# Optimization experiments

Hardware: AMD Instinct MI355X
Metric: run time of the kernel (lower is better)

Reference implementation:

```python
import jax, jax.numpy as jnp
import numpy as np

N, H, E, D, L = 100000, 20000, 1600000, 64, 3
F = 4 * D  # ffn hidden = out_dim * 4


def _ln(x, g, b, eps=1e-5):
    mu = x.mean(-1, keepdims=True)
    var = ((x - mu) ** 2).mean(-1, keepdims=True)
    return (x - mu) * jax.lax.rsqrt(var + eps) * g + b


def _gconv(x, W, b, src, dst, inv_sqrt_src, inv_sqrt_dst, n_dst):
    # DGL GraphConv, norm='both': D_dst^{-1/2} A D_src^{-1/2} (x W) + b
    h = (x * inv_sqrt_src[:, None]) @ W
    agg = jax.ops.segment_sum(h[src], dst, num_segments=n_dst)
    return agg * inv_sqrt_dst[:, None] + b


def setup_inputs() -> dict:
    key = jax.random.key(0)
    ks = jax.random.split(key, 24)
    s = 0.05
    inp = {
        'node_features': jax.random.normal(ks[0], (N, D), jnp.float32),
        'edge_src': jax.random.randint(ks[1], (E,), 0, N),
        'edge_dst': jax.random.randint(ks[2], (E,), 0, H),
        'n_hyper': H,
        # stacked per-layer params [L, ...]
        'Wn2h': jax.random.normal(ks[3], (L, D, D), jnp.float32) * s,
        'bn2h': jnp.zeros((L, D), jnp.float32),
        'Wh2n': jax.random.normal(ks[4], (L, D, D), jnp.float32) * s,
        'bh2n': jnp.zeros((L, D), jnp.float32),
        'W1': jax.random.normal(ks[5], (L, D, F), jnp.float32) * s,
        'b1': jnp.zeros((L, F), jnp.float32),
        'W2': jax.random.normal(ks[6], (L, F, D), jnp.float32) * s,
        'b2': jnp.zeros((L, D), jnp.float32),
        'g1': jnp.ones((L, D), jnp.float32),
        'be1': jnp.zeros((L, D), jnp.float32),
        'g2': jnp.ones((L, D), jnp.float32),
        'be2': jnp.zeros((L, D), jnp.float32),
        'gF': jnp.ones((D,), jnp.float32),
        'bF': jnp.zeros((D,), jnp.float32),
        'Wo': jax.random.normal(ks[7], (D, D), jnp.float32) * s,
        'bo': jnp.zeros((D,), jnp.float32),
    }
    return inp


def reference(node_features, edge_src, edge_dst, n_hyper, Wn2h, bn2h, Wh2n, bh2n,
              W1, b1, W2, b2, g1, be1, g2, be2, gF, bF, Wo, bo):
    n_nodes = node_features.shape[0]
    ones = jnp.ones(edge_src.shape[0], node_features.dtype)
    deg_node = jnp.clip(jax.ops.segment_sum(ones, edge_src, num_segments=n_nodes), 1.0)
    deg_hyp = jnp.clip(jax.ops.segment_sum(ones, edge_dst, num_segments=n_hyper), 1.0)
    is_node = jax.lax.rsqrt(deg_node)  # node out-degree^{-1/2}
    is_hyp = jax.lax.rsqrt(deg_hyp)    # hyperedge in-degree^{-1/2}

    def step(h, p):
        Wa, ba, Wb, bb, w1, c1, w2, c2, gg1, ee1, gg2, ee2 = p
        # node -> hyperedge conv (unused attention output is overwritten in the original)
        h_hyper = _gconv(h, Wa, ba, edge_src, edge_dst, is_node, is_hyp, n_hyper)
        # hyperedge -> node conv on reversed graph (degrees swap roles)
        h_node = _gconv(h_hyper, Wb, bb, edge_dst, edge_src, is_hyp, is_node, n_nodes)
        h = _ln(h + h_node, gg1, ee1)
        h_ffn = jax.nn.relu(h @ w1 + c1) @ w2 + c2
        h = _ln(h + h_ffn, gg2, ee2)
        return h, None

    h, _ = jax.lax.scan(step, node_features,
                        (Wn2h, bn2h, Wh2n, bh2n, W1, b1, W2, b2, g1, be1, g2, be2))
    h = _ln(h, gF, bF)
    return h @ Wo + bo
```

## Files before the change

kernel.cpp:

```cpp
#include <hip/hip_runtime.h>

#define HYP 20000
#define NLAYER 3
#define NB_H 313
#define NB_N 391
#define PT 4096

typedef __attribute__((ext_vector_type(8))) short short8;
typedef __attribute__((ext_vector_type(4))) float floatx4;

static __device__ __forceinline__ unsigned short f2bf(float f){
  union { float f; unsigned u; } v; v.f = f;
  unsigned r = v.u + 0x7FFF + ((v.u >> 16) & 1);
  return (unsigned short)(r >> 16);
}

__global__ __launch_bounds__(256) void k_hist(const int* __restrict__ src,
    const int* __restrict__ dst, int E, int* __restrict__ bh, int* __restrict__ bn){
  __shared__ int lh[NB_H + NB_N];
  int tid = threadIdx.x;
  for (int i = tid; i < NB_H + NB_N; i += 256) lh[i] = 0;
  __syncthreads();
  for (int i = blockIdx.x*256 + tid; i < E; i += gridDim.x*256){
    atomicAdd(&lh[dst[i] >> 6], 1);
    atomicAdd(&lh[NB_H + (src[i] >> 8)], 1);
  }
  __syncthreads();
  for (int i = tid; i < NB_H; i += 256) if (lh[i]) atomicAdd(&bh[i], lh[i]);
  for (int i = tid; i < NB_N; i += 256) if (lh[NB_H+i]) atomicAdd(&bn[i], lh[NB_H+i]);
}

__global__ __launch_bounds__(256) void k_bscan(const int* __restrict__ bh,
    const int* __restrict__ bn, int* __restrict__ bstart_h, int* __restrict__ gcur_h,
    int* __restrict__ bstart_n, int* __restrict__ gcur_n){
  __shared__ int ssc[4];
  __shared__ int scarry;
  int tid = threadIdx.x, lane = tid & 63, wv = tid >> 6;
  if (tid == 0) scarry = 0;
  __syncthreads();
  for (int base = 0; base < NB_H; base += 256){
    int i = base + tid; int v = (i < NB_H) ? bh[i] : 0; int x = v;
    #pragma unroll
    for (int o = 1; o < 64; o <<= 1){ int t = __shfl_up(x,o,64); if (lane >= o) x += t; }
    if (lane == 63) ssc[wv] = x;
    __syncthreads();
    int add = (wv>0?ssc[0]:0)+(wv>1?ssc[1]:0)+(wv>2?ssc[2]:0);
    int c = scarry;
    if (i < NB_H){ int ex = c + add + x - v; bstart_h[i] = ex; gcur_h[i] = ex; }
    __syncthreads();
    if (tid == 255) scarry = c + ssc[0]+ssc[1]+ssc[2]+ssc[3];
    __syncthreads();
  }
  if (tid == 0){ bstart_h[NB_H] = scarry; scarry = 0; }
  __syncthreads();
  for (int base = 0; base < NB_N; base += 256){
    int i = base + tid; int v = (i < NB_N) ? bn[i] : 0; int x = v;
    #pragma unroll
    for (int o = 1; o < 64; o <<= 1){ int t = __shfl_up(x,o,64); if (lane >= o) x += t; }
    if (lane == 63) ssc[wv] = x;
    __syncthreads();
    int add = (wv>0?ssc[0]:0)+(wv>1?ssc[1]:0)+(wv>2?ssc[2]:0);
    int c = scarry;
    if (i < NB_N){ int ex = c + add + x - v; bstart_n[i] = ex; gcur_n[i] = ex; }
    __syncthreads();
    if (tid == 255) scarry = c + ssc[0]+ssc[1]+ssc[2]+ssc[3];
    __syncthreads();
  }
  if (tid == 0) bstart_n[NB_N] = scarry;
}

__global__ __launch_bounds__(256) void k_partition(const int* __restrict__ keys,
    const int* __restrict__ pays, int E, int keyshift, int nb,
    int* __restrict__ gcur, unsigned* __restrict__ Ebuf){
  __shared__ unsigned sst[PT];
  __shared__ int lh[NB_N], lpre[NB_N], gb[NB_N];
  __shared__ int ssc[4];
  __shared__ int scarry;
  int tid = threadIdx.x, lane = tid & 63, wv = tid >> 6;
  int base = blockIdx.x*PT;
  int m = min(PT, E - base);
  for (int i = tid; i < nb; i += 256) lh[i] = 0;
  if (tid == 0) scarry = 0;
  __syncthreads();
  unsigned en[16]; int rk[16];
  #pragma unroll
  for (int j = 0; j < 16; ++j){
    int i = base + j*256 + tid;
    if (i < E){
      unsigned k = (unsigned)keys[i], p = (unsigned)pays[i];
      en[j] = (k << keyshift) | p;
      rk[j] = atomicAdd(&lh[en[j] >> 23], 1);
    } else { en[j] = 0; rk[j] = -1; }
  }
  __syncthreads();
  for (int b2 = 0; b2 < nb; b2 += 256){
    int i = b2 + tid; int v = (i < nb) ? lh[i] : 0; int x = v;
    #pragma unroll
    for (int o = 1; o < 64; o <<= 1){ int t = __shfl_up(x,o,64); if (lane >= o) x += t; }
    if (lane == 63) ssc[wv] = x;
    __syncthreads();
    int add = (wv>0?ssc[0]:0)+(wv>1?ssc[1]:0)+(wv>2?ssc[2]:0);
    int c = scarry;
    if (i < nb) lpre[i] = c + add + x - v;
    __syncthreads();
    if (tid == 255) scarry = c + ssc[0]+ssc[1]+ssc[2]+ssc[3];
    __syncthreads();
  }
  for (int i = tid; i < nb; i += 256) gb[i] = atomicAdd(&gcur[i], lh[i]);
  #pragma unroll
  for (int j = 0; j < 16; ++j){
    if (rk[j] >= 0){
      int bk = en[j] >> 23;
      sst[lpre[bk] + rk[j]] = en[j];
    }
  }
  __syncthreads();
  for (int j = tid; j < m; j += 256){
    unsigned e = sst[j];
    int bk = e >> 23;
    Ebuf[gb[bk] + (j - lpre[bk])] = e;
  }
}

__global__ __launch_bounds__(256) void k_build(const unsigned* __restrict__ Ebuf,
    const int* __restrict__ bstart, int keyshift, int ipb, int paymask, int limit,
    int* __restrict__ off, float* __restrict__ isv, int* __restrict__ csr){
  __shared__ int lcnt[256], lpre2[256], lcur[256];
  int tid = threadIdx.x, lane = tid & 63, wv = tid >> 6;
  int b = blockIdx.x;
  int base = bstart[b], m = bstart[b+1] - base;
  for (int i = tid; i < ipb; i += 256) lcnt[i] = 0;
  __syncthreads();
  for (int i = tid; i < m; i += 256){
    unsigned e = Ebuf[base + i];
    atomicAdd(&lcnt[(e >> keyshift) & (ipb-1)], 1);
  }
  __syncthreads();
  if (wv == 0){
    int carry = 0;
    for (int c = 0; c < ipb; c += 64){
      int li = c + lane;
      int v = lcnt[li]; int x = v;
      #pragma unroll
      for (int o = 1; o < 64; o <<= 1){ int t = __shfl_up(x,o,64); if (lane >= o) x += t; }
      int ex = carry + x - v;
      int id = b*ipb + li;
      if (id <= limit) off[id] = base + ex;
      if (id < limit) isv[id] = rsqrtf((float)(v > 0 ? v : 1));
      lpre2[li] = ex;
      carry += __shfl(x, 63, 64);
    }
  }
  for (int i = tid; i < ipb; i += 256) lcur[i] = 0;
  __syncthreads();
  for (int i = tid; i < m; i += 256){
    unsigned e = Ebuf[base + i];
    int li = (e >> keyshift) & (ipb-1);
    int pos = base + lpre2[li] + atomicAdd(&lcur[li], 1);
    csr[pos] = (int)(e & (unsigned)paymask);
  }
}

__global__ void k_prescale(const float* __restrict__ x, const float* __restrict__ isn,
                           unsigned short* __restrict__ xb, int nrows){
  int i = blockIdx.x*blockDim.x + threadIdx.x;
  int st = gridDim.x*blockDim.x;
  int tot = nrows*8;
  for (; i < tot; i += st){
    float s = isn[i >> 3];
    float4 v0 = *(const float4*)&x[(size_t)i*8];
    float4 v1 = *(const float4*)&x[(size_t)i*8 + 4];
    uint4 o;
    o.x = (unsigned)f2bf(v0.x*s) | ((unsigned)f2bf(v0.y*s) << 16);
    o.y = (unsigned)f2bf(v0.z*s) | ((unsigned)f2bf(v0.w*s) << 16);
    o.z = (unsigned)f2bf(v1.x*s) | ((unsigned)f2bf(v1.y*s) << 16);
    o.w = (unsigned)f2bf(v1.z*s) | ((unsigned)f2bf(v1.w*s) << 16);
    *(uint4*)&xb[(size_t)i*8] = o;
  }
}

__global__ void k_cvtall(const float* __restrict__ W1, const float* __restrict__ W2,
                         const float* __restrict__ Wa, const float* __restrict__ Wb,
                         const float* __restrict__ Wo,
                         unsigned short* __restrict__ W1T, unsigned short* __restrict__ W2T,
                         unsigned short* __restrict__ WaT, unsigned short* __restrict__ WbT,
                         unsigned short* __restrict__ WoT){
  int st = gridDim.x*blockDim.x;
  int t0 = blockIdx.x*blockDim.x + threadIdx.x;
  for (int j = t0; j < NLAYER*16384; j += st){
    int l = j >> 14, n = (j >> 6) & 255, k = j & 63;
    W1T[j] = f2bf(W1[l*16384 + k*256 + n]);
  }
  for (int j = t0; j < NLAYER*16384; j += st){
    int l = j >> 14, o = (j >> 8) & 63, kk = j & 255;
    W2T[j] = f2bf(W2[l*16384 + kk*64 + o]);
  }
  for (int j = t0; j < NLAYER*4096; j += st){
    int l = j >> 12, n = (j >> 6) & 63, k = j & 63;
    WaT[j] = f2bf(Wa[l*4096 + k*64 + n]);
  }
  for (int j = t0; j < NLAYER*4096; j += st){
    int l = j >> 12, n = (j >> 6) & 63, k = j & 63;
    WbT[j] = f2bf(Wb[l*4096 + k*64 + n]);
  }
  for (int j = t0; j < 4096; j += st){
    int n = (j >> 6) & 63, k = j & 63;
    WoT[j] = f2bf(Wo[k*64 + n]);
  }
}

template<int LSTR>
static __device__ __forceinline__ void stage64(const unsigned short* __restrict__ gsrc,
    unsigned short* __restrict__ ldst, int tid, int rows){
  int nch = rows*8;
  for (int idx = tid; idx < nch; idx += 256){
    int row = idx >> 3, kc = (idx & 7)*8;
    uint4 v = *(const uint4*)&gsrc[row*64 + kc];
    *(uint4*)&ldst[row*LSTR + kc] = v;
  }
}

static __device__ __forceinline__ void stage_swz512(const unsigned short* __restrict__ g,
    int gs, unsigned short* __restrict__ l, int tid){
  int row = tid >> 3, s = tid & 7;
  uint4 v = *(const uint4*)&g[row*gs + s*8];
  *(uint4*)&l[(row << 6) + ((((unsigned)(s ^ row)) & 7u) << 3)] = v;
}

static __device__ __forceinline__ short8 rdswz(const unsigned short* __restrict__ l,
    int row, int slot){
  return *(const short8*)&l[(row << 6) + ((((unsigned)(slot ^ row)) & 7u) << 3)];
}

#define ACC8(u) \
  a0 += __uint_as_float(u.x << 16); a1 += __uint_as_float(u.x & 0xFFFF0000u); \
  a2 += __uint_as_float(u.y << 16); a3 += __uint_as_float(u.y & 0xFFFF0000u); \
  a4 += __uint_as_float(u.z << 16); a5 += __uint_as_float(u.z & 0xFFFF0000u); \
  a6 += __uint_as_float(u.w << 16); a7 += __uint_as_float(u.w & 0xFFFF0000u);

__global__ __launch_bounds__(256) void k_gather8(const unsigned short* __restrict__ feat,
    const int* __restrict__ csr, const int* __restrict__ off,
    unsigned short* __restrict__ agg, int nrows){
  int lane = threadIdx.x & 63, wvi = threadIdx.x >> 6;
  int g = lane >> 3;
  int ch = (lane & 7) * 8;
  int r = blockIdx.x*4 + wvi, stride = gridDim.x*4;
  for (; r < nrows; r += stride){
    int b = off[r], e = off[r+1];
    float a0=0,a1=0,a2=0,a3=0,a4=0,a5=0,a6=0,a7=0;
    int t = b;
    for (; t + 32 <= e; t += 32){
      int s0 = csr[t + g];
      int s1 = csr[t + 8 + g];
      int s2 = csr[t + 16 + g];
      int s3 = csr[t + 24 + g];
      uint4 u0 = *(const uint4*)&feat[(size_t)s0*64 + ch];
      uint4 u1 = *(const uint4*)&feat[(size_t)s1*64 + ch];
      uint4 u2 = *(const uint4*)&feat[(size_t)s2*64 + ch];
      uint4 u3 = *(const uint4*)&feat[(size_t)s3*64 + ch];
      ACC8(u0); ACC8(u1); ACC8(u2); ACC8(u3);
    }
    for (; t + 16 <= e; t += 16){
      int s0 = csr[t + g];
      int s1 = csr[t + 8 + g];
      uint4 u0 = *(const uint4*)&feat[(size_t)s0*64 + ch];
      uint4 u1 = *(const uint4*)&feat[(size_t)s1*64 + ch];
      ACC8(u0); ACC8(u1);
    }
    for (; t < e; t += 8){
      int idx = t + g;
      bool valid = idx < e;
      int s = csr[valid ? idx : b];
      uint4 u = *(const uint4*)&feat[(size_t)s*64 + ch];
      if (!valid){ u.x = 0; u.y = 0; u.z = 0; u.w = 0; }
      ACC8(u);
    }
    #pragma unroll
    for (int o = 8; o <= 32; o <<= 1){
      a0 += __shfl_xor(a0,o,64); a1 += __shfl_xor(a1,o,64);
      a2 += __shfl_xor(a2,o,64); a3 += __shfl_xor(a3,o,64);
      a4 += __shfl_xor(a4,o,64); a5 += __shfl_xor(a5,o,64);
      a6 += __shfl_xor(a6,o,64); a7 += __shfl_xor(a7,o,64);
    }
    if (g == 0){
      uint4 w;
      w.x = (unsigned)f2bf(a0) | ((unsigned)f2bf(a1) << 16);
      w.y = (unsigned)f2bf(a2) | ((unsigned)f2bf(a3) << 16);
      w.z = (unsigned)f2bf(a4) | ((unsigned)f2bf(a5) << 16);
      w.w = (unsigned)f2bf(a6) | ((unsigned)f2bf(a7) << 16);
      *(uint4*)&agg[(size_t)r*64 + ch] = w;
    }
  }
}

__global__ __launch_bounds__(64) void k_mmA(const unsigned short* __restrict__ aggb,
    const unsigned short* __restrict__ WaT, const float* __restrict__ bias,
    const float* __restrict__ ihy, unsigned short* __restrict__ ouths, int nrows){
  __shared__ unsigned short sWb[64*72];
  int lane = threadIdx.x;
  int quad = lane >> 4, n16 = lane & 15;
  for (int idx = lane; idx < 512; idx += 64){
    int row = idx >> 3, kc = (idx & 7)*8;
    *(uint4*)&sWb[row*72 + kc] = *(const uint4*)&WaT[row*64 + kc];
  }
  __syncthreads();
  int rowbase = blockIdx.x*16;
  int arow = min(rowbase + n16, nrows-1);
  short8 a0 = *(const short8*)&aggb[(size_t)arow*64 + quad*8];
  short8 a1 = *(const short8*)&aggb[(size_t)arow*64 + 32 + quad*8];
  float ih[4];
  #pragma unroll
  for (int r = 0; r < 4; ++r) ih[r] = ihy[min(rowbase + quad*4 + r, nrows-1)];
  #pragma unroll
  for (int ot = 0; ot < 4; ++ot){
    floatx4 c = (floatx4){0.f,0.f,0.f,0.f};
    short8 b0 = *(const short8*)&sWb[(ot*16+n16)*72 + quad*8];
    short8 b1 = *(const short8*)&sWb[(ot*16+n16)*72 + 32 + quad*8];
    c = __builtin_amdgcn_mfma_f32_16x16x32_bf16(a0, b0, c, 0, 0, 0);
    c = __builtin_amdgcn_mfma_f32_16x16x32_bf16(a1, b1, c, 0, 0, 0);
    float bl = bias[ot*16 + n16];
    #pragma unroll
    for (int r = 0; r < 4; ++r){
      int rr = rowbase + quad*4 + r;
      if (rr < nrows)
        ouths[(size_t)rr*64 + ot*16 + n16] = f2bf(fmaf(c[r], ih[r], bl) * ih[r]);
    }
  }
}

__global__ __launch_bounds__(512) void k_fused(
    const unsigned short* __restrict__ aggb,
    const unsigned short* __restrict__ WbT,
    const float* __restrict__ bbg,
    const float* __restrict__ isn,
    const float* __restrict__ hin,
    const float* __restrict__ g1v, const float* __restrict__ be1v,
    const unsigned short* __restrict__ W1T, const float* __restrict__ b1g,
    const unsigned short* __restrict__ W2T, const float* __restrict__ b2g,
    const float* __restrict__ g2v, const float* __restrict__ be2v,
    float* __restrict__ Outp, unsigned short* __restrict__ Qs, int nrows)
{
  __shared__ unsigned short sWb[64*64];
  __shared__ unsigned short sW1[4*64*64];
  __shared__ unsigned short sW2[4*64*64];
  __shared__ unsigned short sPH[8*16*72];
  int tid = threadIdx.x;
  int lane = tid & 63, w = tid >> 6;
  int quad = lane >> 4, n16 = lane & 15;
  unsigned short* myP = &sPH[w*16*72];

  stage_swz512(WbT, 64, sWb, tid);
  #pragma unroll
  for (int q = 0; q < 4; ++q) stage_swz512(W1T + q*64*64, 64, sW1 + q*4096, tid);
  #pragma unroll
  for (int q = 0; q < 4; ++q) stage_swz512(W2T + q*64, 256, sW2 + q*4096, tid);

  float bbv[4], g1l[4], be1l[4], b2v[4], g2l[4], be2l[4];
  #pragma unroll
  for (int ot = 0; ot < 4; ++ot){
    bbv[ot] = bbg[ot*16 + n16];
    g1l[ot] = g1v[ot*16 + n16];  be1l[ot] = be1v[ot*16 + n16];
    b2v[ot] = b2g[ot*16 + n16];
    g2l[ot] = g2v[ot*16 + n16];  be2l[ot] = be2v[ot*16 + n16];
  }
  float b1v[4][4];
  #pragma unroll
  for (int q = 0; q < 4; ++q)
    #pragma unroll
    for (int c2 = 0; c2 < 4; ++c2)
      b1v[q][c2] = b1g[q*64 + c2*16 + n16];

  __syncthreads();

  int ngrp = (nrows + 15) >> 4;
  int wwid = blockIdx.x*8 + w;
  int nw = gridDim.x*8;

  for (int grp = wwid; grp < ngrp; grp += nw){
    int rb = grp*16;

    int arow = min(rb + n16, nrows-1);
    short8 a0 = *(const short8*)&aggb[(size_t)arow*64 + quad*8];
    short8 a1 = *(const short8*)&aggb[(size_t)arow*64 + 32 + quad*8];

    float pP[4][4];
    float isr[4];
    #pragma unroll
    for (int r = 0; r < 4; ++r) isr[r] = isn[min(rb + quad*4 + r, nrows-1)];
    #pragma unroll
    for (int ot = 0; ot < 4; ++ot){
      floatx4 c = (floatx4){0.f,0.f,0.f,0.f};
      short8 b0 = rdswz(sWb, ot*16+n16, quad);
      short8 b1 = rdswz(sWb, ot*16+n16, 4+quad);
      c = __builtin_amdgcn_mfma_f32_16x16x32_bf16(a0, b0, c, 0, 0, 0);
      c = __builtin_amdgcn_mfma_f32_16x16x32_bf16(a1, b1, c, 0, 0, 0);
      #pragma unroll
      for (int r = 0; r < 4; ++r){
        int rr = min(rb + quad*4 + r, nrows-1);
        pP[ot][r] = fmaf(c[r], isr[r], bbv[ot]) + hin[(size_t)rr*64 + ot*16 + n16];
      }
    }
    #pragma unroll
    for (int r = 0; r < 4; ++r){
      float sv = (pP[0][r] + pP[1][r]) + (pP[2][r] + pP[3][r]);
      float q = fmaf(pP[0][r], pP[0][r], pP[1][r]*pP[1][r]) +
                fmaf(pP[2][r], pP[2][r], pP[3][r]*pP[3][r]);
      #pragma unroll
      for (int o = 8; o >= 1; o >>= 1){
        sv += __shfl_xor(sv, o, 64);
        q  += __shfl_xor(q, o, 64);
      }
      float mu = sv*(1.f/64.f);
      float var = fmaf(-mu, mu, q*(1.f/64.f));
      float rs = rsqrtf(var + 1e-5f);
      #pragma unroll
      for (int ot = 0; ot < 4; ++ot)
        pP[ot][r] = fmaf((pP[ot][r]-mu)*rs, g1l[ot], be1l[ot]);
    }
    #pragma unroll
    for (int ot = 0; ot < 4; ++ot)
      #pragma unroll
      for (int r = 0; r < 4; ++r)
        myP[(quad*4 + r)*72 + ot*16 + n16] = f2bf(pP[ot][r]);
    short8 p0 = *(const short8*)&myP[n16*72 + quad*8];
    short8 p1 = *(const short8*)&myP[n16*72 + 32 + quad*8];

    floatx4 acc2[4];
    #pragma unroll
    for (int t = 0; t < 4; ++t) acc2[t] = (floatx4){0.f,0.f,0.f,0.f};

    #pragma unroll
    for (int q = 0; q < 4; ++q){
      const unsigned short* sA = sW1 + q*4096;
      const unsigned short* sB = sW2 + q*4096;
      #pragma unroll
      for (int ck2 = 0; ck2 < 2; ++ck2){
        #pragma unroll
        for (int nt = 0; nt < 2; ++nt){
          int nl = ck2*32 + nt*16 + n16;
          floatx4 c = (floatx4){0.f,0.f,0.f,0.f};
          short8 b0 = rdswz(sA, nl, quad);
          short8 b1f = rdswz(sA, nl, 4+quad);
          c = __builtin_amdgcn_mfma_f32_16x16x32_bf16(p0, b0, c, 0, 0, 0);
          c = __builtin_amdgcn_mfma_f32_16x16x32_bf16(p1, b1f, c, 0, 0, 0);
          float bb = b1v[q][ck2*2 + nt];
          #pragma unroll
          for (int r = 0; r < 4; ++r){
            float h = fmaxf(c[r] + bb, 0.f);
            myP[(quad*4 + r)*40 + nt*16 + n16] = f2bf(h);
          }
        }
        short8 a2 = *(const short8*)&myP[n16*40 + quad*8];
        #pragma unroll
        for (int ot = 0; ot < 4; ++ot){
          short8 b2f = rdswz(sB, ot*16+n16, ck2*4 + quad);
          acc2[ot] = __builtin_amdgcn_mfma_f32_16x16x32_bf16(a2, b2f, acc2[ot], 0, 0, 0);
        }
      }
    }

    float pre[4][4];
    #pragma unroll
    for (int ot = 0; ot < 4; ++ot)
      #pragma unroll
      for (int r = 0; r < 4; ++r)
        pre[ot][r] = acc2[ot][r] + b2v[ot] + pP[ot][r];
    #pragma unroll
    for (int r = 0; r < 4; ++r){
      float sv = (pre[0][r] + pre[1][r]) + (pre[2][r] + pre[3][r]);
      float q = fmaf(pre[0][r], pre[0][r], pre[1][r]*pre[1][r]) +
                fmaf(pre[2][r], pre[2][r], pre[3][r]*pre[3][r]);
      #pragma unroll
      for (int o = 8; o >= 1; o >>= 1){
        sv += __shfl_xor(sv, o, 64);
        q  += __shfl_xor(q, o, 64);
      }
      float mu = sv*(1.f/64.f);
      float var = fmaf(-mu, mu, q*(1.f/64.f));
      float rs = rsqrtf(var + 1e-5f);
      int rr = rb + quad*4 + r;
      if (rr < nrows){
        float isr2 = isn[rr];
        #pragma unroll
        for (int ot = 0; ot < 4; ++ot){
          float ov = fmaf((pre[ot][r]-mu)*rs, g2l[ot], be2l[ot]);
          Outp[(size_t)rr*64 + ot*16 + n16] = ov;
          Qs[(size_t)rr*64 + ot*16 + n16] = f2bf(ov * isr2);
        }
      }
    }
  }
}

__global__ __launch_bounds__(256) void k_final(const float* __restrict__ Q,
    const unsigned short* __restrict__ WoT, const float* __restrict__ bog,
    const float* __restrict__ gF, const float* __restrict__ bF,
    float* __restrict__ out, int nrows){
  __shared__ unsigned short sWb[64*72];
  int tid = threadIdx.x;
  int lane = tid & 63, w = tid >> 6;
  int quad = lane >> 4, n16 = lane & 15;
  stage64<72>(WoT, sWb, tid, 64);
  __syncthreads();
  int rowbase = blockIdx.x*64 + w*16;
  int arow = min(rowbase + n16, nrows-1);
  float4 q0 = *(const float4*)&Q[(size_t)arow*64 + quad*8];
  float4 q1 = *(const float4*)&Q[(size_t)arow*64 + quad*8 + 4];
  float4 q2 = *(const float4*)&Q[(size_t)arow*64 + 32 + quad*8];
  float4 q3 = *(const float4*)&Q[(size_t)arow*64 + 32 + quad*8 + 4];
  float s = (q0.x+q0.y+q0.z+q0.w) + (q1.x+q1.y+q1.z+q1.w)
          + (q2.x+q2.y+q2.z+q2.w) + (q3.x+q3.y+q3.z+q3.w);
  float qq = (q0.x*q0.x+q0.y*q0.y+q0.z*q0.z+q0.w*q0.w)
           + (q1.x*q1.x+q1.y*q1.y+q1.z*q1.z+q1.w*q1.w)
           + (q2.x*q2.x+q2.y*q2.y+q2.z*q2.z+q2.w*q2.w)
           + (q3.x*q3.x+q3.y*q3.y+q3.z*q3.z+q3.w*q3.w);
  s += __shfl_xor(s, 16, 64);  qq += __shfl_xor(qq, 16, 64);
  s += __shfl_xor(s, 32, 64);  qq += __shfl_xor(qq, 32, 64);
  float mu = s*(1.f/64.f);
  float var = fmaf(-mu, mu, qq*(1.f/64.f));
  float rs = rsqrtf(var + 1e-5f);
  float4 g0 = *(const float4*)&gF[quad*8];
  float4 g1 = *(const float4*)&gF[quad*8 + 4];
  float4 g2 = *(const float4*)&gF[32 + quad*8];
  float4 g3 = *(const float4*)&gF[32 + quad*8 + 4];
  float4 f0 = *(const float4*)&bF[quad*8];
  float4 f1 = *(const float4*)&bF[quad*8 + 4];
  float4 f2 = *(const float4*)&bF[32 + quad*8];
  float4 f3 = *(const float4*)&bF[32 + quad*8 + 4];
  short8 a0, a1;
  a0[0]=f2bf(fmaf((q0.x-mu)*rs, g0.x, f0.x)); a0[1]=f2bf(fmaf((q0.y-mu)*rs, g0.y, f0.y));
  a0[2]=f2bf(fmaf((q0.z-mu)*rs, g0.z, f0.z)); a0[3]=f2bf(fmaf((q0.w-mu)*rs, g0.w, f0.w));
  a0[4]=f2bf(fmaf((q1.x-mu)*rs, g1.x, f1.x)); a0[5]=f2bf(fmaf((q1.y-mu)*rs, g1.y, f1.y));
  a0[6]=f2bf(fmaf((q1.z-mu)*rs, g1.z, f1.z)); a0[7]=f2bf(fmaf((q1.w-mu)*rs, g1.w, f1.w));
  a1[0]=f2bf(fmaf((q2.x-mu)*rs, g2.x, f2.x)); a1[1]=f2bf(fmaf((q2.y-mu)*rs, g2.y, f2.y));
  a1[2]=f2bf(fmaf((q2.z-mu)*rs, g2.z, f2.z)); a1[3]=f2bf(fmaf((q2.w-mu)*rs, g2.w, f2.w));
  a1[4]=f2bf(fmaf((q3.x-mu)*rs, g3.x, f3.x)); a1[5]=f2bf(fmaf((q3.y-mu)*rs, g3.y, f3.y));
  a1[6]=f2bf(fmaf((q3.z-mu)*rs, g3.z, f3.z)); a1[7]=f2bf(fmaf((q3.w-mu)*rs, g3.w, f3.w));
  #pragma unroll
  for (int ot = 0; ot < 4; ++ot){
    floatx4 c = (floatx4){0.f,0.f,0.f,0.f};
    short8 b0 = *(const short8*)&sWb[(ot*16+n16)*72 + quad*8];
    short8 b1 = *(const short8*)&sWb[(ot*16+n16)*72 + 32 + quad*8];
    c = __builtin_amdgcn_mfma_f32_16x16x32_bf16(a0, b0, c, 0, 0, 0);
    c = __builtin_amdgcn_mfma_f32_16x16x32_bf16(a1, b1, c, 0, 0, 0);
    float bol = bog[ot*16 + n16];
    #pragma unroll
    for (int r = 0; r < 4; ++r){
      int rr = rowbase + quad*4 + r;
      if (rr < nrows) out[(size_t)rr*64 + ot*16 + n16] = c[r] + bol;
    }
  }
}

extern "C" void kernel_launch(void* const* d_in, const int* in_sizes, int n_in,
                              void* d_out, int out_size, void* d_ws, size_t ws_size,
                              hipStream_t stream){
  const float* nf   = (const float*)d_in[0];
  const int*   esrc = (const int*)d_in[1];
  const int*   edst = (const int*)d_in[2];
  const float* Wn2h = (const float*)d_in[4];
  const float* bn2h = (const float*)d_in[5];
  const float* Wh2n = (const float*)d_in[6];
  const float* bh2n = (const float*)d_in[7];
  const float* W1   = (const float*)d_in[8];
  const float* b1   = (const float*)d_in[9];
  const float* W2   = (const float*)d_in[10];
  const float* b2   = (const float*)d_in[11];
  const float* g1   = (const float*)d_in[12];
  const float* be1  = (const float*)d_in[13];
  const float* g2   = (const float*)d_in[14];
  const float* be2  = (const float*)d_in[15];
  const float* gF   = (const float*)d_in[16];
  const float* bF   = (const float*)d_in[17];
  const float* Wo   = (const float*)d_in[18];
  const float* bo   = (const float*)d_in[19];
  const int N = in_sizes[0] / 64;
  const int E = in_sizes[1];
  const int H = HYP;
  float* out = (float*)d_out;

  char* w = (char*)d_ws;
  auto carve = [&](size_t bytes) -> char* {
    char* p = w; w += (bytes + 255) & ~(size_t)255; return p;
  };
  int* bh = (int*)carve((size_t)(NB_H + NB_N)*4);
  int* bn = bh + NB_H;
  int* bstart_h = (int*)carve((size_t)(NB_H+1)*4);
  int* gcur_h   = (int*)carve((size_t)NB_H*4);
  int* bstart_n = (int*)carve((size_t)(NB_N+1)*4);
  int* gcur_n   = (int*)carve((size_t)NB_N*4);
  unsigned* Ebuf_h = (unsigned*)carve((size_t)E*4);
  unsigned* Ebuf_n = (unsigned*)carve((size_t)E*4);
  int*   off_h = (int*)carve((size_t)(H+1)*4);
  int*   off_n = (int*)carve((size_t)(N+1)*4);
  float* is_h  = (float*)carve((size_t)H*4);
  float* is_n  = (float*)carve((size_t)N*4);
  int*   csr_h = (int*)carve((size_t)E*4);
  int*   csr_n = (int*)carve((size_t)E*4);
  unsigned short* aggxb = (unsigned short*)carve((size_t)H*64*2);
  unsigned short* agghb = (unsigned short*)carve((size_t)N*64*2);
  float* Qb    = (float*)carve((size_t)N*64*4);
  unsigned short* hhsb = (unsigned short*)carve((size_t)H*64*2);
  unsigned short* xb0  = (unsigned short*)carve((size_t)N*64*2);
  unsigned short* Qs   = (unsigned short*)carve((size_t)N*64*2);
  unsigned short* W1g16 = (unsigned short*)carve((size_t)NLAYER*64*256*2);
  unsigned short* W2g16 = (unsigned short*)carve((size_t)NLAYER*256*64*2);
  unsigned short* Wag16 = (unsigned short*)carve((size_t)NLAYER*4096*2);
  unsigned short* Wbg16 = (unsigned short*)carve((size_t)NLAYER*4096*2);
  unsigned short* Wog16 = (unsigned short*)carve((size_t)4096*2);

  hipMemsetAsync(bh, 0, (size_t)(NB_H + NB_N)*4, stream);
  k_cvtall<<<96, 256, 0, stream>>>(W1, W2, Wn2h, Wh2n, Wo,
                                   W1g16, W2g16, Wag16, Wbg16, Wog16);
  k_hist<<<512, 256, 0, stream>>>(esrc, edst, E, bh, bn);
  k_bscan<<<1, 256, 0, stream>>>(bh, bn, bstart_h, gcur_h, bstart_n, gcur_n);
  k_partition<<<(E + PT - 1)/PT, 256, 0, stream>>>(edst, esrc, E, 17, NB_H, gcur_h, Ebuf_h);
  k_partition<<<(E + PT - 1)/PT, 256, 0, stream>>>(esrc, edst, E, 15, NB_N, gcur_n, Ebuf_n);
  k_build<<<NB_H, 256, 0, stream>>>(Ebuf_h, bstart_h, 17, 64, 0x1FFFF, H, off_h, is_h, csr_h);
  k_build<<<NB_N, 256, 0, stream>>>(Ebuf_n, bstart_n, 15, 256, 0x7FFF, N, off_n, is_n, csr_n);
  k_prescale<<<2048, 256, 0, stream>>>(nf, is_n, xb0, N);

  const int NB64 = (N + 63)/64;
  const int HB16 = (H + 15)/16;
  for (int l = 0; l < NLAYER; ++l){
    const float* hin = (l == 0) ? nf : Qb;
    const unsigned short* hsrc = (l == 0) ? xb0 : Qs;
    k_gather8<<<2048, 256, 0, stream>>>(hsrc, csr_h, off_h, aggxb, H);
    k_mmA<<<HB16, 64, 0, stream>>>(aggxb, Wag16 + l*4096, bn2h + l*64, is_h, hhsb, H);
    k_gather8<<<2048, 256, 0, stream>>>(hhsb, csr_n, off_n, agghb, N);
    k_fused<<<256, 512, 0, stream>>>(agghb, Wbg16 + l*4096, bh2n + l*64, is_n, hin,
                                     g1 + l*64, be1 + l*64,
                                     W1g16 + l*64*256, b1 + l*256,
                                     W2g16 + l*256*64, b2 + l*64,
                                     g2 + l*64, be2 + l*64, Qb, Qs, N);
  }
  k_final<<<NB64, 256, 0, stream>>>(Qb, Wog16, bo, gF, bF, out, N);
}
```

Baseline: 511.5 us.

## Gather two rows per wave concurrently and double k_fused block size

The gather kernel now has each wave process two destination rows at once, with masked 16-edge steps, so more independent feature loads are in flight. The old unrolled 32-edge fast path is replaced by a single masked loop. k_fused moves from 512 to 1024 threads per block with a unified weight-staging loop, which amortises the shared-weight staging over twice as many waves. The risks are extra register pressure, wasted masked loads when the two rows have different degrees, and possible occupancy limits at 1024 threads.

Result: no change. 518.0 us (+1.3%).

```diff
diff --git a/kernel.cpp b/kernel.cpp
--- a/kernel.cpp
+++ b/kernel.cpp
@@ -220,23 +220,21 @@
   }
 }
 
-static __device__ __forceinline__ void stage_swz512(const unsigned short* __restrict__ g,
-    int gs, unsigned short* __restrict__ l, int tid){
-  int row = tid >> 3, s = tid & 7;
-  uint4 v = *(const uint4*)&g[row*gs + s*8];
-  *(uint4*)&l[(row << 6) + ((((unsigned)(s ^ row)) & 7u) << 3)] = v;
-}
-
 static __device__ __forceinline__ short8 rdswz(const unsigned short* __restrict__ l,
     int row, int slot){
   return *(const short8*)&l[(row << 6) + ((((unsigned)(slot ^ row)) & 7u) << 3)];
 }
 
-#define ACC8(u) \
-  a0 += __uint_as_float(u.x << 16); a1 += __uint_as_float(u.x & 0xFFFF0000u); \
-  a2 += __uint_as_float(u.y << 16); a3 += __uint_as_float(u.y & 0xFFFF0000u); \
-  a4 += __uint_as_float(u.z << 16); a5 += __uint_as_float(u.z & 0xFFFF0000u); \
-  a6 += __uint_as_float(u.w << 16); a7 += __uint_as_float(u.w & 0xFFFF0000u);
+#define ACCA(u) \
+  A0 += __uint_as_float(u.x << 16); A1 += __uint_as_float(u.x & 0xFFFF0000u); \
+  A2 += __uint_as_float(u.y << 16); A3 += __uint_as_float(u.y & 0xFFFF0000u); \
+  A4 += __uint_as_float(u.z << 16); A5 += __uint_as_float(u.z & 0xFFFF0000u); \
+  A6 += __uint_as_float(u.w << 16); A7 += __uint_as_float(u.w & 0xFFFF0000u);
+#define ACCB(u) \
+  B0 += __uint_as_float(u.x << 16); B1 += __uint_as_float(u.x & 0xFFFF0000u); \
+  B2 += __uint_as_float(u.y << 16); B3 += __uint_as_float(u.y & 0xFFFF0000u); \
+  B4 += __uint_as_float(u.z << 16); B5 += __uint_as_float(u.z & 0xFFFF0000u); \
+  B6 += __uint_as_float(u.w << 16); B7 += __uint_as_float(u.w & 0xFFFF0000u);
 
 __global__ __launch_bounds__(256) void k_gather8(const unsigned short* __restrict__ feat,
     const int* __restrict__ csr, const int* __restrict__ off,
@@ -244,51 +242,65 @@
   int lane = threadIdx.x & 63, wvi = threadIdx.x >> 6;
   int g = lane >> 3;
   int ch = (lane & 7) * 8;
-  int r = blockIdx.x*4 + wvi, stride = gridDim.x*4;
-  for (; r < nrows; r += stride){
-    int b = off[r], e = off[r+1];
-    float a0=0,a1=0,a2=0,a3=0,a4=0,a5=0,a6=0,a7=0;
-    int t = b;
-    for (; t + 32 <= e; t += 32){
-      int s0 = csr[t + g];
-      int s1 = csr[t + 8 + g];
-      int s2 = csr[t + 16 + g];
-      int s3 = csr[t + 24 + g];
-      uint4 u0 = *(const uint4*)&feat[(size_t)s0*64 + ch];
-      uint4 u1 = *(const uint4*)&feat[(size_t)s1*64 + ch];
-      uint4 u2 = *(const uint4*)&feat[(size_t)s2*64 + ch];
-      uint4 u3 = *(const uint4*)&feat[(size_t)s3*64 + ch];
-      ACC8(u0); ACC8(u1); ACC8(u2); ACC8(u3);
-    }
-    for (; t + 16 <= e; t += 16){
-      int s0 = csr[t + g];
-      int s1 = csr[t + 8 + g];
-      uint4 u0 = *(const uint4*)&feat[(size_t)s0*64 + ch];
-      uint4 u1 = *(const uint4*)&feat[(size_t)s1*64 + ch];
-      ACC8(u0); ACC8(u1);
-    }
-    for (; t < e; t += 8){
-      int idx = t + g;
-      bool valid = idx < e;
-      int s = csr[valid ? idx : b];
-      uint4 u = *(const uint4*)&feat[(size_t)s*64 + ch];
-      if (!valid){ u.x = 0; u.y = 0; u.z = 0; u.w = 0; }
-      ACC8(u);
+  int wid = blockIdx.x*4 + wvi;
+  int nw = gridDim.x*4;
+  for (int r = wid; r < nrows; r += 2*nw){
+    int rA = r;
+    int rB = r + nw;
+    bool hasB = (rB < nrows);
+    int bA = off[rA], eA = off[rA+1];
+    int bB = hasB ? off[rB] : 0;
+    int eB = hasB ? off[rB+1] : 0;
+    float A0=0,A1=0,A2=0,A3=0,A4=0,A5=0,A6=0,A7=0;
+    float B0=0,B1=0,B2=0,B3=0,B4=0,B5=0,B6=0,B7=0;
+    int tA = bA, tB = bB;
+    while (tA < eA || tB < eB){
+      int iA0 = tA + g,     iA1 = tA + 8 + g;
+      int iB0 = tB + g,     iB1 = tB + 8 + g;
+      bool vA0 = iA0 < eA, vA1 = iA1 < eA;
+      bool vB0 = iB0 < eB, vB1 = iB1 < eB;
+      int sA0 = csr[vA0 ? iA0 : 0];
+      int sA1 = csr[vA1 ? iA1 : 0];
+      int sB0 = csr[vB0 ? iB0 : 0];
+      int sB1 = csr[vB1 ? iB1 : 0];
+      uint4 uA0 = *(const uint4*)&feat[(size_t)sA0*64 + ch];
+      uint4 uA1 = *(const uint4*)&feat[(size_t)sA1*64 + ch];
+      uint4 uB0 = *(const uint4*)&feat[(size_t)sB0*64 + ch];
+      uint4 uB1 = *(const uint4*)&feat[(size_t)sB1*64 + ch];
+      if (!vA0){ uA0.x = 0; uA0.y = 0; uA0.z = 0; uA0.w = 0; }
+      if (!vA1){ uA1.x = 0; uA1.y = 0; uA1.z = 0; uA1.w = 0; }
+      if (!vB0){ uB0.x = 0; uB0.y = 0; uB0.z = 0; uB0.w = 0; }
+      if (!vB1){ uB1.x = 0; uB1.y = 0; uB1.z = 0; uB1.w = 0; }
+      ACCA(uA0); ACCA(uA1);
+      ACCB(uB0); ACCB(uB1);
+      tA += 16; tB += 16;
     }
     #pragma unroll
     for (int o = 8; o <= 32; o <<= 1){
-      a0 += __shfl_xor(a0,o,64); a1 += __shfl_xor(a1,o,64);
-      a2 += __shfl_xor(a2,o,64); a3 += __shfl_xor(a3,o,64);
-      a4 += __shfl_xor(a4,o,64); a5 += __shfl_xor(a5,o,64);
-      a6 += __shfl_xor(a6,o,64); a7 += __shfl_xor(a7,o,64);
+      A0 += __shfl_xor(A0,o,64); A1 += __shfl_xor(A1,o,64);
+      A2 += __shfl_xor(A2,o,64); A3 += __shfl_xor(A3,o,64);
+      A4 += __shfl_xor(A4,o,64); A5 += __shfl_xor(A5,o,64);
+      A6 += __shfl_xor(A6,o,64); A7 += __shfl_xor(A7,o,64);
+      B0 += __shfl_xor(B0,o,64); B1 += __shfl_xor(B1,o,64);
+      B2 += __shfl_xor(B2,o,64); B3 += __shfl_xor(B3,o,64);
+      B4 += __shfl_xor(B4,o,64); B5 += __shfl_xor(B5,o,64);
+      B6 += __shfl_xor(B6,o,64); B7 += __shfl_xor(B7,o,64);
     }
     if (g == 0){
       uint4 w;
-      w.x = (unsigned)f2bf(a0) | ((unsigned)f2bf(a1) << 16);
-      w.y = (unsigned)f2bf(a2) | ((unsigned)f2bf(a3) << 16);
-      w.z = (unsigned)f2bf(a4) | ((unsigned)f2bf(a5) << 16);
-      w.w = (unsigned)f2bf(a6) | ((unsigned)f2bf(a7) << 16);
-      *(uint4*)&agg[(size_t)r*64 + ch] = w;
+      w.x = (unsigned)f2bf(A0) | ((unsigned)f2bf(A1) << 16);
+      w.y = (unsigned)f2bf(A2) | ((unsigned)f2bf(A3) << 16);
+      w.z = (unsigned)f2bf(A4) | ((unsigned)f2bf(A5) << 16);
+      w.w = (unsigned)f2bf(A6) | ((unsigned)f2bf(A7) << 16);
+      *(uint4*)&agg[(size_t)rA*64 + ch] = w;
+      if (hasB){
+        uint4 x;
+        x.x = (unsigned)f2bf(B0) | ((unsigned)f2bf(B1) << 16);
+        x.y = (unsigned)f2bf(B2) | ((unsigned)f2bf(B3) << 16);
+        x.z = (unsigned)f2bf(B4) | ((unsigned)f2bf(B5) << 16);
+        x.w = (unsigned)f2bf(B6) | ((unsigned)f2bf(B7) << 16);
+        *(uint4*)&agg[(size_t)rB*64 + ch] = x;
+      }
     }
   }
 }
@@ -328,7 +340,7 @@
   }
 }
 
-__global__ __launch_bounds__(512) void k_fused(
+__global__ __launch_bounds__(1024) void k_fused(
     const unsigned short* __restrict__ aggb,
     const unsigned short* __restrict__ WbT,
     const float* __restrict__ bbg,
@@ -343,17 +355,22 @@
   __shared__ unsigned short sWb[64*64];
   __shared__ unsigned short sW1[4*64*64];
   __shared__ unsigned short sW2[4*64*64];
-  __shared__ unsigned short sPH[8*16*72];
+  __shared__ unsigned short sPH[16*16*72];
   int tid = threadIdx.x;
   int lane = tid & 63, w = tid >> 6;
   int quad = lane >> 4, n16 = lane & 15;
   unsigned short* myP = &sPH[w*16*72];
 
-  stage_swz512(WbT, 64, sWb, tid);
-  #pragma unroll
-  for (int q = 0; q < 4; ++q) stage_swz512(W1T + q*64*64, 64, sW1 + q*4096, tid);
-  #pragma unroll
-  for (int q = 0; q < 4; ++q) stage_swz512(W2T + q*64, 256, sW2 + q*4096, tid);
+  for (int c = tid; c < 4608; c += 1024){
+    int tile = c >> 9, cc = c & 511;
+    int row = cc >> 3, s = cc & 7;
+    const unsigned short* src; unsigned short* dst; int gs;
+    if (tile == 0){ src = WbT; gs = 64; dst = sWb; }
+    else if (tile < 5){ int q = tile-1; src = W1T + q*64*64; gs = 64; dst = sW1 + q*4096; }
+    else { int q = tile-5; src = W2T + q*64; gs = 256; dst = sW2 + q*4096; }
+    uint4 v = *(const uint4*)&src[row*gs + s*8];
+    *(uint4*)&dst[(row << 6) + ((((unsigned)(s ^ row)) & 7u) << 3)] = v;
+  }
 
   float bbv[4], g1l[4], be1l[4], b2v[4], g2l[4], be2l[4];
   #pragma unroll
@@ -373,8 +390,8 @@
   __syncthreads();
 
   int ngrp = (nrows + 15) >> 4;
-  int wwid = blockIdx.x*8 + w;
-  int nw = gridDim.x*8;
+  int wwid = blockIdx.x*16 + w;
+  int nw = gridDim.x*16;
 
   for (int grp = wwid; grp < ngrp; grp += nw){
     int rb = grp*16;
@@ -628,11 +645,11 @@
     k_gather8<<<2048, 256, 0, stream>>>(hsrc, csr_h, off_h, aggxb, H);
     k_mmA<<<HB16, 64, 0, stream>>>(aggxb, Wag16 + l*4096, bn2h + l*64, is_h, hhsb, H);
     k_gather8<<<2048, 256, 0, stream>>>(hhsb, csr_n, off_n, agghb, N);
-    k_fused<<<256, 512, 0, stream>>>(agghb, Wbg16 + l*4096, bh2n + l*64, is_n, hin,
-                                     g1 + l*64, be1 + l*64,
-                                     W1g16 + l*64*256, b1 + l*256,
-                                     W2g16 + l*256*64, b2 + l*64,
-                                     g2 + l*64, be2 + l*64, Qb, Qs, N);
+    k_fused<<<256, 1024, 0, stream>>>(agghb, Wbg16 + l*4096, bh2n + l*64, is_n, hin,
+                                      g1 + l*64, be1 + l*64,
+                                      W1g16 + l*64*256, b1 + l*256,
+                                      W2g16 + l*256*64, b2 + l*64,
+                                      g2 + l*64, be2 + l*64, Qb, Qs, N);
   }
   k_final<<<NB64, 256, 0, stream>>>(Qb, Wog16, bo, gF, bF, out, N);
 }
```
